# Kernel tuning notes

Hardware: AMD Instinct MI355X
Metric: run time of the kernel (lower is better)

The kernel has to match this reference:

```python
import jax, jax.numpy as jnp
import numpy as np

IN_DIM = 1024
K = 8
QK_DIM = IN_DIM // K  # 128


def setup_inputs() -> dict:
    key = jax.random.key(0)
    ks = jax.random.split(key, 8)
    B, C, L = 8, IN_DIM, 2048
    d = QK_DIM
    s_in = 1.0 / np.sqrt(C)  # torch Conv1d default init scale (kaiming-uniform-ish)
    x = jax.random.normal(ks[0], (B, C, L), dtype=jnp.float32)
    Wq = jax.random.uniform(ks[1], (d, C), jnp.float32, -s_in, s_in)
    bq = jax.random.uniform(ks[2], (d,), jnp.float32, -s_in, s_in)
    Wk = jax.random.uniform(ks[3], (d, C), jnp.float32, -s_in, s_in)
    bk = jax.random.uniform(ks[4], (d,), jnp.float32, -s_in, s_in)
    Wv = jax.random.uniform(ks[5], (C, C), jnp.float32, -s_in, s_in)
    bv = jax.random.uniform(ks[6], (C,), jnp.float32, -s_in, s_in)
    gamma = jnp.zeros((1,), dtype=jnp.float32)  # nn.Parameter(torch.zeros(1))
    return {"x": x, "Wq": Wq, "bq": bq, "Wk": Wk, "bk": bk, "Wv": Wv, "bv": bv, "gamma": gamma}


def reference(x, Wq, bq, Wk, bk, Wv, bv, gamma):
    # x: [B, C, L]; 1x1 Conv1d == per-position linear over channels
    q = jnp.einsum("dc,bcl->bld", Wq, x) + bq  # proj_query permuted: [B, L, d]
    k = jnp.einsum("dc,bcl->bdl", Wk, x) + bk[None, :, None]  # [B, d, L]
    v = jnp.einsum("oc,bcl->bol", Wv, x) + bv[None, :, None]  # [B, C, L]
    energy = jnp.einsum("bld,bdm->blm", q, k)  # unscaled attention logits [B, L, L]
    attention = jax.nn.softmax(energy, axis=-1)  # softmax over keys
    # out = bmm(V, attention^T): out[b,c,j] = sum_l attention[b,j,l] * v[b,c,l]
    out = jnp.einsum("bcl,bjl->bcj", v, attention)  # [B, C, L]
    return gamma * out + x
```

## Files before the change

kernel.cpp:

```cpp
#include <hip/hip_runtime.h>
#include <hip/hip_bf16.h>
#include <stdint.h>

#define B_SZ 8
#define C_SZ 1024
#define L_SZ 2048
#define D_SZ 128
#define LOG2E 1.44269504088896f

typedef const float* __restrict__ fpp;
typedef __hip_bfloat16 bf16;
typedef short s8v __attribute__((ext_vector_type(8)));
typedef float f4v __attribute__((ext_vector_type(4)));

#define MFMA __builtin_amdgcn_mfma_f32_16x16x32_bf16

#define GLOAD16(gp, lp) __builtin_amdgcn_global_load_lds(                  \
    (const __attribute__((address_space(1))) void*)(gp),                   \
    (__attribute__((address_space(3))) void*)(lp), 16, 0, 0)

__global__ __launch_bounds__(256) void cast_kernel(fpp src, bf16* __restrict__ dst,
                                                   int n4, float scale) {
  const int i = blockIdx.x * 256 + threadIdx.x;
  if (i < n4) {
    const float4 v = reinterpret_cast<const float4*>(src)[i];
    bf16 o[4] = {__float2bfloat16(v.x * scale), __float2bfloat16(v.y * scale),
                 __float2bfloat16(v.z * scale), __float2bfloat16(v.w * scale)};
    reinterpret_cast<uint2*>(dst)[i] = *reinterpret_cast<uint2*>(o);
  }
}

__global__ __launch_bounds__(256) void bcat_kernel(fpp bq, fpp bk, fpp bv,
                                                   float* __restrict__ bcat) {
  const int i = blockIdx.x * 256 + threadIdx.x;
  if (i < 128)        bcat[i] = bq[i] * LOG2E;
  else if (i < 256)   bcat[i] = bk[i - 128];
  else if (i < 1280)  bcat[i] = bv[i - 256];
}

__global__ __launch_bounds__(256) void transpose_kernel(fpp x, bf16* __restrict__ xT) {
  const int b  = blockIdx.z;
  const int l0 = blockIdx.x * 32;
  const int c0 = blockIdx.y * 32;
  __shared__ float T[32][33];
  const int t = threadIdx.x;
  const int r  = t >> 3;
  const int cg = (t & 7) * 4;
  const float4 v = *reinterpret_cast<const float4*>(
      x + ((size_t)b * C_SZ + c0 + r) * L_SZ + l0 + cg);
  T[r][cg + 0] = v.x; T[r][cg + 1] = v.y; T[r][cg + 2] = v.z; T[r][cg + 3] = v.w;
  __syncthreads();
  bf16 o[4];
#pragma unroll
  for (int i = 0; i < 4; ++i) o[i] = __float2bfloat16(T[cg + i][r]);
  *reinterpret_cast<uint2*>(
      xT + ((size_t)b * L_SZ + l0 + r) * C_SZ + c0 + cg) = *reinterpret_cast<uint2*>(o);
}

__global__ __launch_bounds__(256) void proj_kernel(
    const bf16* __restrict__ xTb, const bf16* __restrict__ Wcat, fpp bcat,
    bf16* __restrict__ Qt, bf16* __restrict__ Kt, bf16* __restrict__ Vt) {
  __shared__ bf16 Als[128 * 64];
  __shared__ bf16 Bls[128 * 64];
  const int bid = blockIdx.x;
  const int tid = threadIdx.x, wid = tid >> 6, lane = tid & 63;
  const int lm = lane & 15, lg = lane >> 4;
  const int wm = wid >> 1, wn = wid & 1;
  const bool isQK = bid < 256;

  const bf16 *Arow, *Brow;
  int m0, n0;
  if (isQK) {
    m0 = (bid & 1) * 128;
    n0 = (bid >> 1) * 128;
    Arow = Wcat; Brow = xTb;
  } else {
    const int v = bid - 256;
    m0 = (v >> 3) * 128;
    n0 = (v & 7) * 128;
    Arow = xTb; Brow = Wcat + (size_t)256 * C_SZ;
  }

  const int srow = lane >> 3;
  const int scol = (lane & 7) * 8;

  f4v acc[4][4] = {};
  for (int k0 = 0; k0 < C_SZ; k0 += 64) {
    __syncthreads();
#pragma unroll
    for (int ch = 0; ch < 4; ++ch) {
      const int chunk = wid * 4 + ch;
      const int row = chunk * 8 + srow;
      GLOAD16(Arow + (size_t)(m0 + row) * C_SZ + k0 + scol, &Als[chunk * 512]);
      GLOAD16(Brow + (size_t)(n0 + row) * C_SZ + k0 + scol, &Bls[chunk * 512]);
    }
    __syncthreads();
#pragma unroll
    for (int kc = 0; kc < 2; ++kc) {
      s8v af[4], bfr[4];
#pragma unroll
      for (int i = 0; i < 4; ++i) {
        af[i]  = *reinterpret_cast<const s8v*>(
            &Als[(wm * 64 + i * 16 + lm) * 64 + kc * 32 + lg * 8]);
        bfr[i] = *reinterpret_cast<const s8v*>(
            &Bls[(wn * 64 + i * 16 + lm) * 64 + kc * 32 + lg * 8]);
      }
#pragma unroll
      for (int a = 0; a < 4; ++a)
#pragma unroll
        for (int bj = 0; bj < 4; ++bj)
          acc[a][bj] = MFMA(af[a], bfr[bj], acc[a][bj], 0, 0, 0);
    }
  }

  if (isQK) {
    bf16* dst = (m0 == 0) ? Qt : Kt;
#pragma unroll
    for (int a = 0; a < 4; ++a) {
      const int d = m0 + wm * 64 + a * 16 + lg * 4;
      const int dd = d & 127;
      const float4 bb = *reinterpret_cast<const float4*>(bcat + d);
#pragma unroll
      for (int bj = 0; bj < 4; ++bj) {
        const int gl = n0 + wn * 64 + bj * 16 + lm;
        bf16 o[4] = {__float2bfloat16(acc[a][bj][0] + bb.x),
                     __float2bfloat16(acc[a][bj][1] + bb.y),
                     __float2bfloat16(acc[a][bj][2] + bb.z),
                     __float2bfloat16(acc[a][bj][3] + bb.w)};
        *reinterpret_cast<uint2*>(dst + (size_t)gl * D_SZ + dd) =
            *reinterpret_cast<uint2*>(o);
      }
    }
  } else {
#pragma unroll
    for (int a = 0; a < 4; ++a) {
      const int gl = m0 + wm * 64 + a * 16 + lg * 4;
      const int b = gl >> 11, l = gl & 2047;
#pragma unroll
      for (int bj = 0; bj < 4; ++bj) {
        const int c = n0 + wn * 64 + bj * 16 + lm;
        const float bvc = bcat[256 + c];
        bf16 o[4] = {__float2bfloat16(acc[a][bj][0] + bvc),
                     __float2bfloat16(acc[a][bj][1] + bvc),
                     __float2bfloat16(acc[a][bj][2] + bvc),
                     __float2bfloat16(acc[a][bj][3] + bvc)};
        *reinterpret_cast<uint2*>(Vt + ((size_t)b * C_SZ + c) * L_SZ + l) =
            *reinterpret_cast<uint2*>(o);
      }
    }
  }
}

__global__ __launch_bounds__(256) void pv_kernel(
    const bf16* __restrict__ Qt, const bf16* __restrict__ Kt,
    const bf16* __restrict__ Vt,
    fpp x, fpp gamma, float* __restrict__ out) {
  const int gid = blockIdx.x;
  const int b  = gid & 7;
  const int ct = (gid >> 3) & 3;
  const int qt = gid >> 5;
  const int j0 = qt * 64;
  const int c0 = ct * 256;
  const int tid = threadIdx.x, wid = tid >> 6, lane = tid & 63;
  const int lm = lane & 15, lg = lane >> 4;

  __shared__ bf16 Plds[2][64][64];
  __shared__ float lred[4][4][16];
  __shared__ float linv_lds[64];
  char* const Pbase = (char*)&Plds[0][0][0];

  const int swz = (lm & 7) << 4;
  const int wr_off = (wid * 32 + lg * 8) ^ swz;

  s8v bQ[4][4];
#pragma unroll
  for (int nq = 0; nq < 4; ++nq)
#pragma unroll
    for (int dc = 0; dc < 4; ++dc)
      bQ[nq][dc] = *reinterpret_cast<const s8v*>(
          Qt + ((size_t)b * L_SZ + j0 + nq * 16 + lm) * D_SZ + dc * 32 + lg * 8);

  f4v acc[4][4] = {};
  float lsum[4] = {0.f, 0.f, 0.f, 0.f};
  const bf16* Vbase = Vt + ((size_t)b * C_SZ + c0 + wid * 64) * L_SZ;
  const bf16* Kbase = Kt + (size_t)b * L_SZ * D_SZ;

  int cur = 0;
  for (int k0 = 0; k0 < L_SZ; k0 += 64) {
    s8v vfrag[2][4];
#pragma unroll
    for (int kc = 0; kc < 2; ++kc)
#pragma unroll
      for (int nt = 0; nt < 4; ++nt)
        vfrag[kc][nt] = *reinterpret_cast<const s8v*>(
            Vbase + (size_t)(nt * 16 + lm) * L_SZ + k0 + kc * 32 + lg * 8);

    f4v s[4] = {};
#pragma unroll
    for (int dc = 0; dc < 4; ++dc) {
      const s8v aK = *reinterpret_cast<const s8v*>(
          Kbase + (size_t)(k0 + wid * 16 + lm) * D_SZ + dc * 32 + lg * 8);
#pragma unroll
      for (int nq = 0; nq < 4; ++nq)
        s[nq] = MFMA(aK, bQ[nq][dc], s[nq], 0, 0, 0);
    }

#pragma unroll
    for (int nq = 0; nq < 4; ++nq) {
      bf16 pb[4];
#pragma unroll
      for (int r = 0; r < 4; ++r) {
        const float pf = exp2f(s[nq][r]);
        lsum[nq] += pf;
        pb[r] = __float2bfloat16(pf);
      }
      *reinterpret_cast<uint2*>(
          Pbase + cur * 8192 + (nq * 16 + lm) * 128 + wr_off) =
          *reinterpret_cast<uint2*>(pb);
    }
    __syncthreads();

#pragma unroll
    for (int kc = 0; kc < 2; ++kc) {
      const int rd_off = (kc * 64 + lg * 16) ^ swz;
      s8v aP[4];
#pragma unroll
      for (int mq = 0; mq < 4; ++mq)
        aP[mq] = *reinterpret_cast<const s8v*>(
            Pbase + cur * 8192 + (mq * 16 + lm) * 128 + rd_off);
#pragma unroll
      for (int nt = 0; nt < 4; ++nt)
#pragma unroll
        for (int mq = 0; mq < 4; ++mq)
          acc[mq][nt] = MFMA(aP[mq], vfrag[kc][nt], acc[mq][nt], 0, 0, 0);
    }
    cur ^= 1;
  }

#pragma unroll
  for (int nq = 0; nq < 4; ++nq) {
    lsum[nq] += __shfl_xor(lsum[nq], 16);
    lsum[nq] += __shfl_xor(lsum[nq], 32);
  }
  if (lg == 0) {
#pragma unroll
    for (int nq = 0; nq < 4; ++nq) lred[wid][nq][lm] = lsum[nq];
  }
  __syncthreads();
  if (tid < 64) {
    const int nq = tid >> 4, l2 = tid & 15;
    linv_lds[tid] = 1.0f /
        (lred[0][nq][l2] + lred[1][nq][l2] + lred[2][nq][l2] + lred[3][nq][l2]);
  }
  __syncthreads();

  const float g = gamma[0];
#pragma unroll
  for (int mq = 0; mq < 4; ++mq) {
    float li[4];
#pragma unroll
    for (int r = 0; r < 4; ++r) li[r] = linv_lds[mq * 16 + lg * 4 + r];
#pragma unroll
    for (int nt = 0; nt < 4; ++nt) {
      const int c = c0 + wid * 64 + nt * 16 + lm;
      const int j = j0 + mq * 16 + lg * 4;
      const size_t off = ((size_t)b * C_SZ + c) * L_SZ + j;
      const float4 xv = *reinterpret_cast<const float4*>(x + off);
      float4 o;
      o.x = g * (acc[mq][nt][0] * li[0]) + xv.x;
      o.y = g * (acc[mq][nt][1] * li[1]) + xv.y;
      o.z = g * (acc[mq][nt][2] * li[2]) + xv.z;
      o.w = g * (acc[mq][nt][3] * li[3]) + xv.w;
      *reinterpret_cast<float4*>(out + off) = o;
    }
  }
}

extern "C" void kernel_launch(void* const* d_in, const int* in_sizes, int n_in,
                              void* d_out, int out_size, void* d_ws,
                              size_t ws_size, hipStream_t stream) {
  fpp x     = (fpp)d_in[0];
  fpp Wq    = (fpp)d_in[1];
  fpp bq    = (fpp)d_in[2];
  fpp Wk    = (fpp)d_in[3];
  fpp bk    = (fpp)d_in[4];
  fpp Wv    = (fpp)d_in[5];
  fpp bv    = (fpp)d_in[6];
  fpp gamma = (fpp)d_in[7];
  float* out = (float*)d_out;

  bf16* xTb  = (bf16*)d_out;
  bf16* Wcat = xTb + (size_t)B_SZ * L_SZ * C_SZ;
  bf16* Qt = (bf16*)d_ws;
  bf16* Kt = Qt + (size_t)B_SZ * L_SZ * D_SZ;
  bf16* Vt = Kt + (size_t)B_SZ * L_SZ * D_SZ;
  float* bcat = (float*)(Vt + (size_t)B_SZ * C_SZ * L_SZ);

  const dim3 blk(256);
  cast_kernel<<<dim3(128), blk, 0, stream>>>(Wq, Wcat, D_SZ * C_SZ / 4, LOG2E);
  cast_kernel<<<dim3(128), blk, 0, stream>>>(Wk, Wcat + (size_t)D_SZ * C_SZ,
                                             D_SZ * C_SZ / 4, 1.0f);
  cast_kernel<<<dim3(1024), blk, 0, stream>>>(Wv, Wcat + (size_t)2 * D_SZ * C_SZ,
                                              C_SZ * C_SZ / 4, 1.0f);
  bcat_kernel<<<dim3(5), blk, 0, stream>>>(bq, bk, bv, bcat);
  transpose_kernel<<<dim3(L_SZ / 32, C_SZ / 32, B_SZ), blk, 0, stream>>>(x, xTb);
  proj_kernel<<<dim3(256 + 1024), blk, 0, stream>>>(xTb, Wcat, bcat, Qt, Kt, Vt);
  pv_kernel<<<dim3(B_SZ * 4 * (L_SZ / 64)), blk, 0, stream>>>(
      Qt, Kt, Vt, x, gamma, out);
}
```

Before: 305.9 us.

## Fuse weight-prep kernels, stage Q in LDS, prefetch K, cheaper exp/bf16 packing

Merges the three weight cast launches and the bias launch into one prep kernel. In the attention kernel, Q is staged into swizzled LDS instead of 16 held register fragments, which frees registers. K fragments for the next tile are double-buffered in registers and prefetched one iteration ahead. The exp2 now uses the hardware builtin with manual round-to-nearest bf16 packing, and the PV MFMA phase runs at raised wave priority. The trade-offs are extra LDS traffic for Q reads on every tile and a slightly different bf16 rounding of the probabilities (NaN and tie handling differ).

```diff
diff --git a/kernel.cpp b/kernel.cpp
--- a/kernel.cpp
+++ b/kernel.cpp
@@ -19,23 +19,26 @@
     (const __attribute__((address_space(1))) void*)(gp),                   \
     (__attribute__((address_space(3))) void*)(lp), 16, 0, 0)
 
-__global__ __launch_bounds__(256) void cast_kernel(fpp src, bf16* __restrict__ dst,
-                                                   int n4, float scale) {
-  const int i = blockIdx.x * 256 + threadIdx.x;
-  if (i < n4) {
-    const float4 v = reinterpret_cast<const float4*>(src)[i];
+__global__ __launch_bounds__(256) void prep_kernel(
+    fpp Wq, fpp Wk, fpp Wv, fpp bq, fpp bk, fpp bv,
+    bf16* __restrict__ Wcat, float* __restrict__ bcat) {
+  const int bidx = blockIdx.x;
+  if (bidx < 1280) {
+    fpp src; float scale = 1.0f;
+    if (bidx < 128)      { src = Wq + (size_t)bidx * C_SZ; scale = LOG2E; }
+    else if (bidx < 256) { src = Wk + (size_t)(bidx - 128) * C_SZ; }
+    else                 { src = Wv + (size_t)(bidx - 256) * C_SZ; }
+    const float4 v = reinterpret_cast<const float4*>(src)[threadIdx.x];
     bf16 o[4] = {__float2bfloat16(v.x * scale), __float2bfloat16(v.y * scale),
                  __float2bfloat16(v.z * scale), __float2bfloat16(v.w * scale)};
-    reinterpret_cast<uint2*>(dst)[i] = *reinterpret_cast<uint2*>(o);
-  }
-}
-
-__global__ __launch_bounds__(256) void bcat_kernel(fpp bq, fpp bk, fpp bv,
-                                                   float* __restrict__ bcat) {
-  const int i = blockIdx.x * 256 + threadIdx.x;
-  if (i < 128)        bcat[i] = bq[i] * LOG2E;
-  else if (i < 256)   bcat[i] = bk[i - 128];
-  else if (i < 1280)  bcat[i] = bv[i - 256];
+    reinterpret_cast<uint2*>(Wcat + (size_t)bidx * C_SZ)[threadIdx.x] =
+        *reinterpret_cast<uint2*>(o);
+  } else {
+    const int i = (bidx - 1280) * 256 + threadIdx.x;
+    if (i < 128)        bcat[i] = bq[i] * LOG2E;
+    else if (i < 256)   bcat[i] = bk[i - 128];
+    else if (i < 1280)  bcat[i] = bv[i - 256];
+  }
 }
 
 __global__ __launch_bounds__(256) void transpose_kernel(fpp x, bf16* __restrict__ xT) {
@@ -165,77 +168,102 @@
   const int lm = lane & 15, lg = lane >> 4;
 
   __shared__ bf16 Plds[2][64][64];
+  __shared__ bf16 Qlds[64][128];
   __shared__ float lred[4][4][16];
   __shared__ float linv_lds[64];
   char* const Pbase = (char*)&Plds[0][0][0];
+  char* const Qbase = (char*)&Qlds[0][0];
 
   const int swz = (lm & 7) << 4;
   const int wr_off = (wid * 32 + lg * 8) ^ swz;
 
-  s8v bQ[4][4];
-#pragma unroll
-  for (int nq = 0; nq < 4; ++nq)
-#pragma unroll
-    for (int dc = 0; dc < 4; ++dc)
-      bQ[nq][dc] = *reinterpret_cast<const s8v*>(
-          Qt + ((size_t)b * L_SZ + j0 + nq * 16 + lm) * D_SZ + dc * 32 + lg * 8);
+  {
+    const int r  = tid >> 2;
+    const int cb = (tid & 3) * 64;
+    const bf16* src = Qt + ((size_t)b * L_SZ + j0 + r) * D_SZ + cb / 2;
+#pragma unroll
+    for (int j = 0; j < 4; ++j) {
+      const s8v w = *reinterpret_cast<const s8v*>(src + j * 8);
+      const int co = cb + j * 16;
+      *reinterpret_cast<s8v*>(Qbase + r * 256 + (co ^ ((r & 15) << 4))) = w;
+    }
+  }
 
   f4v acc[4][4] = {};
   float lsum[4] = {0.f, 0.f, 0.f, 0.f};
+  s8v kbA[4], kbB[4];
   const bf16* Vbase = Vt + ((size_t)b * C_SZ + c0 + wid * 64) * L_SZ;
   const bf16* Kbase = Kt + (size_t)b * L_SZ * D_SZ;
 
-  int cur = 0;
-  for (int k0 = 0; k0 < L_SZ; k0 += 64) {
-    s8v vfrag[2][4];
-#pragma unroll
-    for (int kc = 0; kc < 2; ++kc)
-#pragma unroll
-      for (int nt = 0; nt < 4; ++nt)
-        vfrag[kc][nt] = *reinterpret_cast<const s8v*>(
-            Vbase + (size_t)(nt * 16 + lm) * L_SZ + k0 + kc * 32 + lg * 8);
-
-    f4v s[4] = {};
-#pragma unroll
-    for (int dc = 0; dc < 4; ++dc) {
-      const s8v aK = *reinterpret_cast<const s8v*>(
-          Kbase + (size_t)(k0 + wid * 16 + lm) * D_SZ + dc * 32 + lg * 8);
-#pragma unroll
-      for (int nq = 0; nq < 4; ++nq)
-        s[nq] = MFMA(aK, bQ[nq][dc], s[nq], 0, 0, 0);
-    }
-
-#pragma unroll
-    for (int nq = 0; nq < 4; ++nq) {
-      bf16 pb[4];
-#pragma unroll
-      for (int r = 0; r < 4; ++r) {
-        const float pf = exp2f(s[nq][r]);
-        lsum[nq] += pf;
-        pb[r] = __float2bfloat16(pf);
-      }
-      *reinterpret_cast<uint2*>(
-          Pbase + cur * 8192 + (nq * 16 + lm) * 128 + wr_off) =
-          *reinterpret_cast<uint2*>(pb);
-    }
-    __syncthreads();
-
-#pragma unroll
-    for (int kc = 0; kc < 2; ++kc) {
-      const int rd_off = (kc * 64 + lg * 16) ^ swz;
-      s8v aP[4];
-#pragma unroll
-      for (int mq = 0; mq < 4; ++mq)
-        aP[mq] = *reinterpret_cast<const s8v*>(
-            Pbase + cur * 8192 + (mq * 16 + lm) * 128 + rd_off);
-#pragma unroll
-      for (int nt = 0; nt < 4; ++nt)
-#pragma unroll
-        for (int mq = 0; mq < 4; ++mq)
-          acc[mq][nt] = MFMA(aP[mq], vfrag[kc][nt], acc[mq][nt], 0, 0, 0);
-    }
-    cur ^= 1;
-  }
+#pragma unroll
+  for (int dc = 0; dc < 4; ++dc)
+    kbA[dc] = *reinterpret_cast<const s8v*>(
+        Kbase + (size_t)(wid * 16 + lm) * D_SZ + dc * 32 + lg * 8);
+  __syncthreads();
+
+#define PV_ITER(nn, KCUR, KNXT)                                                \
+  {                                                                            \
+    const int n = (nn);                                                        \
+    const int k0 = n * 64;                                                     \
+    const int slot = (nn) & 1;                                                 \
+                               \
+    s8v vfrag[2][4];                                                           \
+    _Pragma("unroll") for (int kc = 0; kc < 2; ++kc)                           \
+      _Pragma("unroll") for (int nt = 0; nt < 4; ++nt)                         \
+        vfrag[kc][nt] = *reinterpret_cast<const s8v*>(                         \
+            Vbase + (size_t)(nt * 16 + lm) * L_SZ + k0 + kc * 32 + lg * 8);    \
+                                    \
+    if (n + 1 < 32) {                                                          \
+      _Pragma("unroll") for (int dc = 0; dc < 4; ++dc)                         \
+        KNXT[dc] = *reinterpret_cast<const s8v*>(                              \
+            Kbase + (size_t)(k0 + 64 + wid * 16 + lm) * D_SZ + dc * 32 + lg * 8); \
+    }                                                                          \
+                                \
+    f4v s[4] = {};                                                             \
+    _Pragma("unroll") for (int dc = 0; dc < 4; ++dc) {                         \
+      _Pragma("unroll") for (int nq = 0; nq < 4; ++nq) {                       \
+        const int row = nq * 16 + lm;                                          \
+        const s8v bQf = *reinterpret_cast<const s8v*>(                         \
+            Qbase + row * 256 + ((dc * 64 + lg * 16) ^ ((row & 15) << 4)));    \
+        s[nq] = MFMA(KCUR[dc], bQf, s[nq], 0, 0, 0);                           \
+      }                                                                        \
+    }                                                                          \
+                       \
+    _Pragma("unroll") for (int nq = 0; nq < 4; ++nq) {                         \
+      float p0 = __builtin_amdgcn_exp2f(s[nq][0]);                             \
+      float p1 = __builtin_amdgcn_exp2f(s[nq][1]);                             \
+      float p2 = __builtin_amdgcn_exp2f(s[nq][2]);                             \
+      float p3 = __builtin_amdgcn_exp2f(s[nq][3]);                             \
+      lsum[nq] += (p0 + p1) + (p2 + p3);                                       \
+      uint2 pw;                                                                \
+      pw.x = ((__float_as_uint(p0) + 0x8000u) >> 16) |                         \
+             ((__float_as_uint(p1) + 0x8000u) & 0xFFFF0000u);                  \
+      pw.y = ((__float_as_uint(p2) + 0x8000u) >> 16) |                         \
+             ((__float_as_uint(p3) + 0x8000u) & 0xFFFF0000u);                  \
+      *reinterpret_cast<uint2*>(                                               \
+          Pbase + slot * 8192 + (nq * 16 + lm) * 128 + wr_off) = pw;           \
+    }                                                                          \
+    __syncthreads();                                                           \
+                        \
+    __builtin_amdgcn_s_setprio(1);                                             \
+    _Pragma("unroll") for (int kc = 0; kc < 2; ++kc) {                         \
+      const int rd_off = (kc * 64 + lg * 16) ^ swz;                            \
+      s8v aP[4];                                                               \
+      _Pragma("unroll") for (int mq = 0; mq < 4; ++mq)                         \
+        aP[mq] = *reinterpret_cast<const s8v*>(                                \
+            Pbase + slot * 8192 + (mq * 16 + lm) * 128 + rd_off);              \
+      _Pragma("unroll") for (int nt = 0; nt < 4; ++nt)                         \
+        _Pragma("unroll") for (int mq = 0; mq < 4; ++mq)                       \
+          acc[mq][nt] = MFMA(aP[mq], vfrag[kc][nt], acc[mq][nt], 0, 0, 0);     \
+    }                                                                          \
+    __builtin_amdgcn_s_setprio(0);                                             \
+  }
+
+  for (int it = 0; it < 16; ++it) {
+    PV_ITER(2 * it,     kbA, kbB);
+    PV_ITER(2 * it + 1, kbB, kbA);
+  }
+#undef PV_ITER
 
 #pragma unroll
   for (int nq = 0; nq < 4; ++nq) {
@@ -297,12 +325,7 @@
   float* bcat = (float*)(Vt + (size_t)B_SZ * C_SZ * L_SZ);
 
   const dim3 blk(256);
-  cast_kernel<<<dim3(128), blk, 0, stream>>>(Wq, Wcat, D_SZ * C_SZ / 4, LOG2E);
-  cast_kernel<<<dim3(128), blk, 0, stream>>>(Wk, Wcat + (size_t)D_SZ * C_SZ,
-                                             D_SZ * C_SZ / 4, 1.0f);
-  cast_kernel<<<dim3(1024), blk, 0, stream>>>(Wv, Wcat + (size_t)2 * D_SZ * C_SZ,
-                                              C_SZ * C_SZ / 4, 1.0f);
-  bcat_kernel<<<dim3(5), blk, 0, stream>>>(bq, bk, bv, bcat);
+  prep_kernel<<<dim3(1285), blk, 0, stream>>>(Wq, Wk, Wv, bq, bk, bv, Wcat, bcat);
   transpose_kernel<<<dim3(L_SZ / 32, C_SZ / 32, B_SZ), blk, 0, stream>>>(x, xTb);
   proj_kernel<<<dim3(256 + 1024), blk, 0, stream>>>(xTb, Wcat, bcat, Qt, Kt, Vt);
   pv_kernel<<<dim3(B_SZ * 4 * (L_SZ / 64)), blk, 0, stream>>>(
```

After: 299.2 us. 1.02x faster.
